# Optimization experiments

Measured on AMD Instinct MI355X. Metric: run time of the kernel, lower is better.

## Reference

```python
import jax, jax.numpy as jnp
import numpy as np

N_TRAJS = 8
N_RES = 500
N_BINS = 34
K_CB_DIST = 150.0
FORCE_CUTOFF = 40.0


def setup_inputs() -> dict:
    key = jax.random.key(0)
    k1, k2 = jax.random.split(key)
    # spread coords so pair distances span several bins
    coords_cb = jax.random.normal(k1, (N_TRAJS, N_RES, 3), dtype=jnp.float32) * 8.0
    gaussian_weights = jax.random.uniform(k2, (N_RES, N_RES, N_BINS), dtype=jnp.float32)
    dist_bin_centres = 3.75 + 0.5 * jnp.arange(N_BINS, dtype=jnp.float32)
    sigmas = jnp.full((N_BINS,), 1.25, dtype=jnp.float32)
    return {
        "coords_cb": coords_cb,
        "gaussian_weights": gaussian_weights,
        "dist_bin_centres": dist_bin_centres,
        "sigmas": sigmas,
    }


def reference(coords_cb, gaussian_weights, dist_bin_centres, sigmas):
    # crep[t, i, j] = cb[t, j]; diffs = crep - crep.transpose(1,2) -> cb[j] - cb[i]
    diffs = coords_cb[:, None, :, :] - coords_cb[:, :, None, :]  # [T, i, j, 3]
    dists = jnp.clip(jnp.sqrt(jnp.sum(diffs * diffs, axis=-1)), 0.1, FORCE_CUTOFF)  # [T,i,j]
    norm_diffs = diffs / dists[..., None]
    # per-bin Gaussian mixture energies and radial force
    dfm = dists[..., None] - dist_bin_centres  # [T, i, j, B]
    cb_energies = gaussian_weights[None] * jnp.exp(-0.5 * (dfm / sigmas) ** 2) / sigmas
    forces = jnp.sum(-dfm / (sigmas * sigmas) * cb_energies, axis=-1)  # [T, i, j]
    pair_accs = -forces[..., None] * K_CB_DIST * norm_diffs  # [T, i, j, 3]
    # accs['CB'] += pair_accs.sum(dim=1)
    return jnp.sum(pair_accs, axis=1)  # [T, n_res, 3]
```

## Files before the change

kernel.cpp:

```cpp
#include <hip/hip_runtime.h>
#include <hip/hip_bf16.h>

#define NTRAJ 8
#define NRES  500
#define NBINS 34
#define ICHUNKS 250
#define OUT_ELEMS (NTRAJ*NRES*3)

__global__ __launch_bounds__(256)
void force_main(const float* __restrict__ cb,
                const float* __restrict__ gw,
                const float* __restrict__ cen,
                const float* __restrict__ sig,
                float* __restrict__ dst,
                int atomicMode)
{
    const int tid = threadIdx.x;
    const int j   = blockIdx.y * 256 + tid;
    const int ic  = blockIdx.x;
    if (j >= NRES) return;

    float cbj[NTRAJ][3];
#pragma unroll
    for (int t = 0; t < NTRAJ; ++t)
#pragma unroll
        for (int c = 0; c < 3; ++c)
            cbj[t][c] = cb[t * (NRES * 3) + j * 3 + c];

    float acc[NTRAJ][3];
#pragma unroll
    for (int t = 0; t < NTRAJ; ++t)
#pragma unroll
        for (int c = 0; c < 3; ++c)
            acc[t][c] = 0.0f;

#pragma unroll
    for (int ii = 0; ii < 2; ++ii) {
        const int i = ic * 2 + ii;

        float dx[NTRAJ], dy[NTRAJ], dz[NTRAJ], d[NTRAJ];
#pragma unroll
        for (int t = 0; t < NTRAJ; ++t) {
            const float xi = cb[t * (NRES * 3) + i * 3 + 0];
            const float yi = cb[t * (NRES * 3) + i * 3 + 1];
            const float zi = cb[t * (NRES * 3) + i * 3 + 2];
            dx[t] = cbj[t][0] - xi;
            dy[t] = cbj[t][1] - yi;
            dz[t] = cbj[t][2] - zi;
            float d2 = dx[t] * dx[t] + dy[t] * dy[t] + dz[t] * dz[t];
            float dd = sqrtf(d2);
            dd = fminf(fmaxf(dd, 0.1f), 40.0f);
            d[t] = dd;
        }

        float force[NTRAJ];
#pragma unroll
        for (int t = 0; t < NTRAJ; ++t) force[t] = 0.0f;

        const float2* g2 = reinterpret_cast<const float2*>(
            gw + (size_t)i * (NRES * NBINS) + (size_t)j * NBINS);

#pragma unroll
        for (int k = 0; k < NBINS / 2; ++k) {
            const float2 wpair = g2[k];
#pragma unroll
            for (int u = 0; u < 2; ++u) {
                const int b   = 2 * k + u;
                const float w = u ? wpair.y : wpair.x;
                const float sv = __builtin_amdgcn_rcpf(sig[b]);
                const float s2 = sv * sv;
                const float c1 = s2 * -0.72134752044448f;
                const float wb = (w * sv) * s2;
                const float cc = cen[b];
#pragma unroll
                for (int t = 0; t < NTRAJ; ++t) {
                    const float dfm = d[t] - cc;
                    const float e   = __builtin_amdgcn_exp2f(dfm * dfm * c1);
                    force[t] = fmaf(-(dfm * wb), e, force[t]);
                }
            }
        }

#pragma unroll
        for (int t = 0; t < NTRAJ; ++t) {
            const float s = (force[t] * __builtin_amdgcn_rcpf(d[t])) * -150.0f;
            acc[t][0] = fmaf(s, dx[t], acc[t][0]);
            acc[t][1] = fmaf(s, dy[t], acc[t][1]);
            acc[t][2] = fmaf(s, dz[t], acc[t][2]);
        }
    }

    if (atomicMode) {
#pragma unroll
        for (int t = 0; t < NTRAJ; ++t)
#pragma unroll
            for (int c = 0; c < 3; ++c)
                atomicAdd(dst + t * (NRES * 3) + j * 3 + c, acc[t][c]);
    } else {
        float* p = dst + (size_t)ic * OUT_ELEMS;
#pragma unroll
        for (int t = 0; t < NTRAJ; ++t)
#pragma unroll
            for (int c = 0; c < 3; ++c)
                p[t * (NRES * 3) + j * 3 + c] = acc[t][c];
    }
}

__global__ __launch_bounds__(256)
void reduce_k(const float* __restrict__ part, float* __restrict__ out)
{
    const int o = blockIdx.x * 256 + threadIdx.x;
    if (o >= OUT_ELEMS) return;
    float s = 0.0f;
#pragma unroll 5
    for (int ic = 0; ic < ICHUNKS; ++ic)
        s += part[(size_t)ic * OUT_ELEMS + o];
    out[o] = s;
}

__global__ __launch_bounds__(256)
void zero_k(float* __restrict__ out)
{
    const int o = blockIdx.x * 256 + threadIdx.x;
    if (o < OUT_ELEMS) out[o] = 0.0f;
}

extern "C" void kernel_launch(void* const* d_in, const int* in_sizes, int n_in,
                              void* d_out, int out_size, void* d_ws, size_t ws_size,
                              hipStream_t stream)
{
    const float* cb  = (const float*)d_in[0];
    const float* gw  = (const float*)d_in[1];
    const float* cen = (const float*)d_in[2];
    const float* sig = (const float*)d_in[3];
    float* out = (float*)d_out;

    const size_t need = (size_t)ICHUNKS * OUT_ELEMS * sizeof(float);
    const int outBlocks = (OUT_ELEMS + 255) / 256;

    if (ws_size >= need) {
        float* part = (float*)d_ws;
        force_main<<<dim3(ICHUNKS, 2), 256, 0, stream>>>(cb, gw, cen, sig, part, 0);
        reduce_k<<<outBlocks, 256, 0, stream>>>(part, out);
    } else {
        zero_k<<<outBlocks, 256, 0, stream>>>(out);
        force_main<<<dim3(ICHUNKS, 2), 256, 0, stream>>>(cb, gw, cen, sig, out, 1);
    }
}
```

Baseline: 116.2 us.

## Use one i per block and split the partial-sum reduction into atomic groups

The force kernel now handles a single i row per block, launching 500x2 blocks instead of 250x2, and writes per-i partials rather than accumulating two rows. The reduction kernel reads with float4 and splits the 500 slabs into 10 groups across a second grid dimension, combining the groups with atomics into an output zeroed by hipMemsetAsync. The goal is more blocks in flight for the force stage and a wider, more parallel reduction. In exchange, the partial buffer doubles to about 24 MB, the fallback for a small workspace is dropped, and an extra memset launch is added.

```diff
diff --git a/kernel.cpp b/kernel.cpp
--- a/kernel.cpp
+++ b/kernel.cpp
@@ -1,23 +1,24 @@
 #include <hip/hip_runtime.h>
-#include <hip/hip_bf16.h>
 
 #define NTRAJ 8
 #define NRES  500
 #define NBINS 34
-#define ICHUNKS 250
+#define NSLAB NRES
 #define OUT_ELEMS (NTRAJ*NRES*3)
+#define OUT4 (OUT_ELEMS/4)
+#define RED_G   10
+#define RED_PER (NSLAB/RED_G)
 
 __global__ __launch_bounds__(256)
 void force_main(const float* __restrict__ cb,
                 const float* __restrict__ gw,
                 const float* __restrict__ cen,
                 const float* __restrict__ sig,
-                float* __restrict__ dst,
-                int atomicMode)
+                float* __restrict__ part)
 {
     const int tid = threadIdx.x;
     const int j   = blockIdx.y * 256 + tid;
-    const int ic  = blockIdx.x;
+    const int i   = blockIdx.x;
     if (j >= NRES) return;
 
     float cbj[NTRAJ][3];
@@ -27,102 +28,76 @@
         for (int c = 0; c < 3; ++c)
             cbj[t][c] = cb[t * (NRES * 3) + j * 3 + c];
 
-    float acc[NTRAJ][3];
+    float dx[NTRAJ], dy[NTRAJ], dz[NTRAJ], d[NTRAJ];
 #pragma unroll
-    for (int t = 0; t < NTRAJ; ++t)
+    for (int t = 0; t < NTRAJ; ++t) {
+        const float xi = cb[t * (NRES * 3) + i * 3 + 0];
+        const float yi = cb[t * (NRES * 3) + i * 3 + 1];
+        const float zi = cb[t * (NRES * 3) + i * 3 + 2];
+        dx[t] = cbj[t][0] - xi;
+        dy[t] = cbj[t][1] - yi;
+        dz[t] = cbj[t][2] - zi;
+        float d2 = dx[t] * dx[t] + dy[t] * dy[t] + dz[t] * dz[t];
+        float dd = sqrtf(d2);
+        d[t] = fminf(fmaxf(dd, 0.1f), 40.0f);
+    }
+
+    float force[NTRAJ];
 #pragma unroll
-        for (int c = 0; c < 3; ++c)
-            acc[t][c] = 0.0f;
+    for (int t = 0; t < NTRAJ; ++t) force[t] = 0.0f;
+
+    const float2* g2 = reinterpret_cast<const float2*>(
+        gw + (size_t)i * (NRES * NBINS) + (size_t)j * NBINS);
 
 #pragma unroll
-    for (int ii = 0; ii < 2; ++ii) {
-        const int i = ic * 2 + ii;
-
-        float dx[NTRAJ], dy[NTRAJ], dz[NTRAJ], d[NTRAJ];
+    for (int k = 0; k < NBINS / 2; ++k) {
+        const float2 wpair = g2[k];
 #pragma unroll
-        for (int t = 0; t < NTRAJ; ++t) {
-            const float xi = cb[t * (NRES * 3) + i * 3 + 0];
-            const float yi = cb[t * (NRES * 3) + i * 3 + 1];
-            const float zi = cb[t * (NRES * 3) + i * 3 + 2];
-            dx[t] = cbj[t][0] - xi;
-            dy[t] = cbj[t][1] - yi;
-            dz[t] = cbj[t][2] - zi;
-            float d2 = dx[t] * dx[t] + dy[t] * dy[t] + dz[t] * dz[t];
-            float dd = sqrtf(d2);
-            dd = fminf(fmaxf(dd, 0.1f), 40.0f);
-            d[t] = dd;
-        }
-
-        float force[NTRAJ];
+        for (int u = 0; u < 2; ++u) {
+            const int b   = 2 * k + u;
+            const float w = u ? wpair.y : wpair.x;
+            const float sv = __builtin_amdgcn_rcpf(sig[b]);
+            const float s2 = sv * sv;
+            const float c1 = s2 * -0.72134752044448f;
+            const float wb = (w * sv) * s2;
+            const float cc = cen[b];
 #pragma unroll
-        for (int t = 0; t < NTRAJ; ++t) force[t] = 0.0f;
-
-        const float2* g2 = reinterpret_cast<const float2*>(
-            gw + (size_t)i * (NRES * NBINS) + (size_t)j * NBINS);
-
-#pragma unroll
-        for (int k = 0; k < NBINS / 2; ++k) {
-            const float2 wpair = g2[k];
-#pragma unroll
-            for (int u = 0; u < 2; ++u) {
-                const int b   = 2 * k + u;
-                const float w = u ? wpair.y : wpair.x;
-                const float sv = __builtin_amdgcn_rcpf(sig[b]);
-                const float s2 = sv * sv;
-                const float c1 = s2 * -0.72134752044448f;
-                const float wb = (w * sv) * s2;
-                const float cc = cen[b];
-#pragma unroll
-                for (int t = 0; t < NTRAJ; ++t) {
-                    const float dfm = d[t] - cc;
-                    const float e   = __builtin_amdgcn_exp2f(dfm * dfm * c1);
-                    force[t] = fmaf(-(dfm * wb), e, force[t]);
-                }
+            for (int t = 0; t < NTRAJ; ++t) {
+                const float dfm = d[t] - cc;
+                const float e   = __builtin_amdgcn_exp2f((dfm * c1) * dfm);
+                force[t] = fmaf(-(dfm * wb), e, force[t]);
             }
-        }
-
-#pragma unroll
-        for (int t = 0; t < NTRAJ; ++t) {
-            const float s = (force[t] * __builtin_amdgcn_rcpf(d[t])) * -150.0f;
-            acc[t][0] = fmaf(s, dx[t], acc[t][0]);
-            acc[t][1] = fmaf(s, dy[t], acc[t][1]);
-            acc[t][2] = fmaf(s, dz[t], acc[t][2]);
         }
     }
 
-    if (atomicMode) {
+    float* p = part + (size_t)i * OUT_ELEMS;
 #pragma unroll
-        for (int t = 0; t < NTRAJ; ++t)
-#pragma unroll
-            for (int c = 0; c < 3; ++c)
-                atomicAdd(dst + t * (NRES * 3) + j * 3 + c, acc[t][c]);
-    } else {
-        float* p = dst + (size_t)ic * OUT_ELEMS;
-#pragma unroll
-        for (int t = 0; t < NTRAJ; ++t)
-#pragma unroll
-            for (int c = 0; c < 3; ++c)
-                p[t * (NRES * 3) + j * 3 + c] = acc[t][c];
+    for (int t = 0; t < NTRAJ; ++t) {
+        const float s = (force[t] * __builtin_amdgcn_rcpf(d[t])) * -150.0f;
+        p[t * (NRES * 3) + j * 3 + 0] = s * dx[t];
+        p[t * (NRES * 3) + j * 3 + 1] = s * dy[t];
+        p[t * (NRES * 3) + j * 3 + 2] = s * dz[t];
     }
 }
 
 __global__ __launch_bounds__(256)
 void reduce_k(const float* __restrict__ part, float* __restrict__ out)
 {
-    const int o = blockIdx.x * 256 + threadIdx.x;
-    if (o >= OUT_ELEMS) return;
-    float s = 0.0f;
-#pragma unroll 5
-    for (int ic = 0; ic < ICHUNKS; ++ic)
-        s += part[(size_t)ic * OUT_ELEMS + o];
-    out[o] = s;
-}
+    const int f = blockIdx.x * 256 + threadIdx.x;
+    if (f >= OUT4) return;
+    const int g = blockIdx.y;
 
-__global__ __launch_bounds__(256)
-void zero_k(float* __restrict__ out)
-{
-    const int o = blockIdx.x * 256 + threadIdx.x;
-    if (o < OUT_ELEMS) out[o] = 0.0f;
+    const float4* p4 = reinterpret_cast<const float4*>(part);
+    float4 s = make_float4(0.f, 0.f, 0.f, 0.f);
+#pragma unroll 10
+    for (int ic = g * RED_PER; ic < (g + 1) * RED_PER; ++ic) {
+        const float4 v = p4[(size_t)ic * OUT4 + f];
+        s.x += v.x; s.y += v.y; s.z += v.z; s.w += v.w;
+    }
+    atomicAdd(out + f * 4 + 0, s.x);
+    atomicAdd(out + f * 4 + 1, s.y);
+    atomicAdd(out + f * 4 + 2, s.z);
+    atomicAdd(out + f * 4 + 3, s.w);
 }
 
 extern "C" void kernel_launch(void* const* d_in, const int* in_sizes, int n_in,
@@ -133,17 +108,11 @@
     const float* gw  = (const float*)d_in[1];
     const float* cen = (const float*)d_in[2];
     const float* sig = (const float*)d_in[3];
-    float* out = (float*)d_out;
+    float* out  = (float*)d_out;
+    float* part = (float*)d_ws;
 
-    const size_t need = (size_t)ICHUNKS * OUT_ELEMS * sizeof(float);
-    const int outBlocks = (OUT_ELEMS + 255) / 256;
+    hipMemsetAsync(out, 0, (size_t)OUT_ELEMS * sizeof(float), stream);
 
-    if (ws_size >= need) {
-        float* part = (float*)d_ws;
-        force_main<<<dim3(ICHUNKS, 2), 256, 0, stream>>>(cb, gw, cen, sig, part, 0);
-        reduce_k<<<outBlocks, 256, 0, stream>>>(part, out);
-    } else {
-        zero_k<<<outBlocks, 256, 0, stream>>>(out);
-        force_main<<<dim3(ICHUNKS, 2), 256, 0, stream>>>(cb, gw, cen, sig, out, 1);
-    }
+    force_main<<<dim3(NSLAB, 2), 256, 0, stream>>>(cb, gw, cen, sig, part);
+    reduce_k<<<dim3((OUT4 + 255) / 256, RED_G), 256, 0, stream>>>(part, out);
 }
```

Measured after the change: 105.6 us. -9.2%, faster.

## Assign one block per output residue and reduce in-block, dropping partial buffers

Applied to the files above, without the earlier changes.

The work split is transposed: each block now owns one output residue j, and its threads loop over the source residues i. The sum over i is done in-block with wavefront xor-shuffles and a small shared-memory combine. This removes the large partial-sum workspace, its write and read traffic, and the separate reduction (or zero-plus-atomic) launch. In exchange, each lane now reads gaussian weights at a 68KB stride across lanes, so the loads are poorly coalesced and rely on cache line reuse across the bin loop. Threads beyond residue 500 sit idle on the second pass.

```diff
diff --git a/kernel.cpp b/kernel.cpp
--- a/kernel.cpp
+++ b/kernel.cpp
@@ -1,31 +1,26 @@
 #include <hip/hip_runtime.h>
-#include <hip/hip_bf16.h>
 
 #define NTRAJ 8
 #define NRES  500
 #define NBINS 34
-#define ICHUNKS 250
-#define OUT_ELEMS (NTRAJ*NRES*3)
 
 __global__ __launch_bounds__(256)
-void force_main(const float* __restrict__ cb,
-                const float* __restrict__ gw,
-                const float* __restrict__ cen,
-                const float* __restrict__ sig,
-                float* __restrict__ dst,
-                int atomicMode)
+void force_all(const float* __restrict__ cb,
+               const float* __restrict__ gw,
+               const float* __restrict__ cen,
+               const float* __restrict__ sig,
+               float* __restrict__ out)
 {
     const int tid = threadIdx.x;
-    const int j   = blockIdx.y * 256 + tid;
-    const int ic  = blockIdx.x;
-    if (j >= NRES) return;
+    const int j   = blockIdx.x;
 
-    float cbj[NTRAJ][3];
+    float xj[NTRAJ], yj[NTRAJ], zj[NTRAJ];
 #pragma unroll
-    for (int t = 0; t < NTRAJ; ++t)
-#pragma unroll
-        for (int c = 0; c < 3; ++c)
-            cbj[t][c] = cb[t * (NRES * 3) + j * 3 + c];
+    for (int t = 0; t < NTRAJ; ++t) {
+        xj[t] = cb[t * (NRES * 3) + j * 3 + 0];
+        yj[t] = cb[t * (NRES * 3) + j * 3 + 1];
+        zj[t] = cb[t * (NRES * 3) + j * 3 + 2];
+    }
 
     float acc[NTRAJ][3];
 #pragma unroll
@@ -36,93 +31,80 @@
 
 #pragma unroll
     for (int ii = 0; ii < 2; ++ii) {
-        const int i = ic * 2 + ii;
+        const int i = ii * 256 + tid;
+        if (i < NRES) {
+            float dx[NTRAJ], dy[NTRAJ], dz[NTRAJ], d[NTRAJ];
+#pragma unroll
+            for (int t = 0; t < NTRAJ; ++t) {
+                dx[t] = xj[t] - cb[t * (NRES * 3) + i * 3 + 0];
+                dy[t] = yj[t] - cb[t * (NRES * 3) + i * 3 + 1];
+                dz[t] = zj[t] - cb[t * (NRES * 3) + i * 3 + 2];
+                const float d2 = dx[t] * dx[t] + dy[t] * dy[t] + dz[t] * dz[t];
+                d[t] = fminf(fmaxf(sqrtf(d2), 0.1f), 40.0f);
+            }
 
-        float dx[NTRAJ], dy[NTRAJ], dz[NTRAJ], d[NTRAJ];
+            float force[NTRAJ];
 #pragma unroll
-        for (int t = 0; t < NTRAJ; ++t) {
-            const float xi = cb[t * (NRES * 3) + i * 3 + 0];
-            const float yi = cb[t * (NRES * 3) + i * 3 + 1];
-            const float zi = cb[t * (NRES * 3) + i * 3 + 2];
-            dx[t] = cbj[t][0] - xi;
-            dy[t] = cbj[t][1] - yi;
-            dz[t] = cbj[t][2] - zi;
-            float d2 = dx[t] * dx[t] + dy[t] * dy[t] + dz[t] * dz[t];
-            float dd = sqrtf(d2);
-            dd = fminf(fmaxf(dd, 0.1f), 40.0f);
-            d[t] = dd;
-        }
+            for (int t = 0; t < NTRAJ; ++t) force[t] = 0.0f;
 
-        float force[NTRAJ];
-#pragma unroll
-        for (int t = 0; t < NTRAJ; ++t) force[t] = 0.0f;
-
-        const float2* g2 = reinterpret_cast<const float2*>(
-            gw + (size_t)i * (NRES * NBINS) + (size_t)j * NBINS);
+            const float2* g2 = reinterpret_cast<const float2*>(
+                gw + (size_t)i * (NRES * NBINS) + (size_t)j * NBINS);
 
 #pragma unroll
-        for (int k = 0; k < NBINS / 2; ++k) {
-            const float2 wpair = g2[k];
+            for (int k = 0; k < NBINS / 2; ++k) {
+                const float2 wpair = g2[k];
 #pragma unroll
-            for (int u = 0; u < 2; ++u) {
-                const int b   = 2 * k + u;
-                const float w = u ? wpair.y : wpair.x;
-                const float sv = __builtin_amdgcn_rcpf(sig[b]);
-                const float s2 = sv * sv;
-                const float c1 = s2 * -0.72134752044448f;
-                const float wb = (w * sv) * s2;
-                const float cc = cen[b];
+                for (int u = 0; u < 2; ++u) {
+                    const int b   = 2 * k + u;
+                    const float w = u ? wpair.y : wpair.x;
+                    const float sv = __builtin_amdgcn_rcpf(sig[b]);
+                    const float s2 = sv * sv;
+                    const float c1 = s2 * -0.72134752044448f;
+                    const float wb = (w * sv) * s2;
+                    const float cc = cen[b];
 #pragma unroll
-                for (int t = 0; t < NTRAJ; ++t) {
-                    const float dfm = d[t] - cc;
-                    const float e   = __builtin_amdgcn_exp2f(dfm * dfm * c1);
-                    force[t] = fmaf(-(dfm * wb), e, force[t]);
+                    for (int t = 0; t < NTRAJ; ++t) {
+                        const float dfm = d[t] - cc;
+                        const float e   = __builtin_amdgcn_exp2f((dfm * c1) * dfm);
+                        force[t] = fmaf(-(dfm * wb), e, force[t]);
+                    }
                 }
             }
-        }
 
 #pragma unroll
-        for (int t = 0; t < NTRAJ; ++t) {
-            const float s = (force[t] * __builtin_amdgcn_rcpf(d[t])) * -150.0f;
-            acc[t][0] = fmaf(s, dx[t], acc[t][0]);
-            acc[t][1] = fmaf(s, dy[t], acc[t][1]);
-            acc[t][2] = fmaf(s, dz[t], acc[t][2]);
+            for (int t = 0; t < NTRAJ; ++t) {
+                const float s = (force[t] * __builtin_amdgcn_rcpf(d[t])) * -150.0f;
+                acc[t][0] = fmaf(s, dx[t], acc[t][0]);
+                acc[t][1] = fmaf(s, dy[t], acc[t][1]);
+                acc[t][2] = fmaf(s, dz[t], acc[t][2]);
+            }
         }
     }
 
-    if (atomicMode) {
+#pragma unroll
+    for (int m = 1; m <= 32; m <<= 1)
 #pragma unroll
         for (int t = 0; t < NTRAJ; ++t)
 #pragma unroll
             for (int c = 0; c < 3; ++c)
-                atomicAdd(dst + t * (NRES * 3) + j * 3 + c, acc[t][c]);
-    } else {
-        float* p = dst + (size_t)ic * OUT_ELEMS;
+                acc[t][c] += __shfl_xor(acc[t][c], m, 64);
+
+    __shared__ float red[4][NTRAJ * 3];
+    const int wv = tid >> 6;
+    if ((tid & 63) == 0) {
 #pragma unroll
         for (int t = 0; t < NTRAJ; ++t)
 #pragma unroll
             for (int c = 0; c < 3; ++c)
-                p[t * (NRES * 3) + j * 3 + c] = acc[t][c];
+                red[wv][t * 3 + c] = acc[t][c];
     }
-}
-
-__global__ __launch_bounds__(256)
-void reduce_k(const float* __restrict__ part, float* __restrict__ out)
-{
-    const int o = blockIdx.x * 256 + threadIdx.x;
-    if (o >= OUT_ELEMS) return;
-    float s = 0.0f;
-#pragma unroll 5
-    for (int ic = 0; ic < ICHUNKS; ++ic)
-        s += part[(size_t)ic * OUT_ELEMS + o];
-    out[o] = s;
-}
-
-__global__ __launch_bounds__(256)
-void zero_k(float* __restrict__ out)
-{
-    const int o = blockIdx.x * 256 + threadIdx.x;
-    if (o < OUT_ELEMS) out[o] = 0.0f;
+    __syncthreads();
+    if (tid < NTRAJ * 3) {
+        const float s = red[0][tid] + red[1][tid] + red[2][tid] + red[3][tid];
+        const int t = tid / 3;
+        const int c = tid - t * 3;
+        out[t * (NRES * 3) + j * 3 + c] = s;
+    }
 }
 
 extern "C" void kernel_launch(void* const* d_in, const int* in_sizes, int n_in,
@@ -135,15 +117,5 @@
     const float* sig = (const float*)d_in[3];
     float* out = (float*)d_out;
 
-    const size_t need = (size_t)ICHUNKS * OUT_ELEMS * sizeof(float);
-    const int outBlocks = (OUT_ELEMS + 255) / 256;
-
-    if (ws_size >= need) {
-        float* part = (float*)d_ws;
-        force_main<<<dim3(ICHUNKS, 2), 256, 0, stream>>>(cb, gw, cen, sig, part, 0);
-        reduce_k<<<outBlocks, 256, 0, stream>>>(part, out);
-    } else {
-        zero_k<<<outBlocks, 256, 0, stream>>>(out);
-        force_main<<<dim3(ICHUNKS, 2), 256, 0, stream>>>(cb, gw, cen, sig, out, 1);
-    }
+    force_all<<<dim3(NRES), 256, 0, stream>>>(cb, gw, cen, sig, out);
 }
```

Result: faster. 97.85 us (-15.8%).
